# Kernel tuning notes

Hardware: AMD Instinct MI355X
Metric: run time of the kernel (lower is better)

Reference implementation:

```python
import jax, jax.numpy as jnp
import numpy as np

N, HID, MAXD, B, NCLS, GRUH = 50000, 128, 16, 50, 10, 32


def setup_inputs() -> dict:
    key = jax.random.key(0)
    ks = jax.random.split(key, 18)
    s = 0.05
    nrm = lambda k, shp: (jax.random.normal(k, shp, jnp.float32) * s)
    return {
        "feature": jax.random.normal(ks[0], (N, HID), jnp.float32),
        "nbr_idx": jax.random.randint(ks[1], (N, MAXD), 0, N, dtype=jnp.int32),
        "deg": jax.random.randint(ks[2], (N,), 1, MAXD + 1, dtype=jnp.int32),
        "graph_ids": (jnp.arange(N, dtype=jnp.int32) * B) // N,
        # SAGEConv(lstm) params: LSTM(in=HID, hidden=HID) + fc_self/fc_neigh
        "lstm_Wih": nrm(ks[3], (4 * HID, HID)),
        "lstm_Whh": nrm(ks[4], (4 * HID, HID)),
        "lstm_bih": nrm(ks[5], (4 * HID,)),
        "lstm_bhh": nrm(ks[6], (4 * HID,)),
        "W_self": nrm(ks[7], (HID, HID)),
        "W_neigh": nrm(ks[8], (HID, HID)),
        "b_sage": nrm(ks[9], (HID,)),
        # GraphConv params
        "W_gc": nrm(ks[10], (HID, HID)),
        "b_gc": nrm(ks[11], (HID,)),
        # GRU params (h0=0 so weight_hh contributes nothing; only its bias matters)
        "Wih_gru": nrm(ks[12], (3 * GRUH, HID)),
        "bih_gru": nrm(ks[13], (3 * GRUH,)),
        "bhh_gru": nrm(ks[14], (3 * GRUH,)),
        # classifier (dropout is identity at eval)
        "W_cls": nrm(ks[15], (GRUH, NCLS)),
        "b_cls": nrm(ks[16], (NCLS,)),
    }


def _lstm_aggregate(feats, nbr_idx, deg, Wih, Whh, bih, bhh):
    # DGL SAGEConv 'lstm' reducer: run LSTM over each node's neighbor features,
    # take final hidden state. Implemented as a masked scan over padded lists.
    n, hdim = feats.shape
    h0 = jnp.zeros((n, hdim), feats.dtype)

    def step(carry, t):
        h, c = carry
        x = feats[jnp.take(nbr_idx, t, axis=1)]  # [N, HID] gather of t-th neighbor
        gates = x @ Wih.T + bih + h @ Whh.T + bhh
        i, f, g, o = jnp.split(gates, 4, axis=-1)  # torch gate order i,f,g,o
        c_new = jax.nn.sigmoid(f) * c + jax.nn.sigmoid(i) * jnp.tanh(g)
        h_new = jax.nn.sigmoid(o) * jnp.tanh(c_new)
        valid = (t < deg)[:, None]
        return (jnp.where(valid, h_new, h), jnp.where(valid, c_new, c)), None

    (hT, _), _ = jax.lax.scan(step, (h0, h0), jnp.arange(nbr_idx.shape[1]))
    return hT  # hidden at each node's last valid neighbor


def _graph_conv(h, nbr_idx, deg, W, b):
    # DGL GraphConv norm='both': D^-1/2 A D^-1/2 h W + b
    n, maxd = nbr_idx.shape
    norm = jax.lax.rsqrt(jnp.maximum(deg.astype(h.dtype), 1.0))
    hn = h * norm[:, None]
    mask = (jnp.arange(maxd, dtype=jnp.int32)[None, :] < deg[:, None]).astype(h.dtype)
    contrib = hn[nbr_idx.reshape(-1)] * mask.reshape(-1)[:, None]  # [N*MAXD, HID]
    dst = jnp.repeat(jnp.arange(n, dtype=jnp.int32), maxd)
    agg = jax.ops.segment_sum(contrib, dst, num_segments=n)
    return (agg * norm[:, None]) @ W + b


def _gru_step(x, Wih, bih, bhh):
    # single GRU step with h0 = 0 (seq_len == 1 in the original view(1, N, H))
    gh = x @ Wih.T + bih  # [N, 3*GRUH]
    xr, xz, xn = jnp.split(gh, 3, axis=-1)  # torch gate order r,z,n
    br, bz, bn = jnp.split(bhh, 3)
    r = jax.nn.sigmoid(xr + br)
    z = jax.nn.sigmoid(xz + bz)
    nst = jnp.tanh(xn + r * bn)
    return (1.0 - z) * nst  # h' = (1-z)*n + z*h0, h0 = 0


def reference(feature, nbr_idx, deg, graph_ids, lstm_Wih, lstm_Whh, lstm_bih,
              lstm_bhh, W_self, W_neigh, b_sage, W_gc, b_gc, Wih_gru, bih_gru,
              bhh_gru, W_cls, b_cls):
    # conv4: SAGEConv lstm -> relu
    h_nei = _lstm_aggregate(feature, nbr_idx, deg, lstm_Wih, lstm_Whh, lstm_bih, lstm_bhh)
    h = jax.nn.relu(feature @ W_self + h_nei @ W_neigh + b_sage)
    # conv2: GraphConv -> relu
    h = jax.nn.relu(_graph_conv(h, nbr_idx, deg, W_gc, b_gc))
    # GRU over seq_len=1, batch=N
    out = _gru_step(h, Wih_gru, bih_gru, bhh_gru)  # [N, 32]
    # dgl.mean_nodes: per-graph mean pool
    sums = jax.ops.segment_sum(out, graph_ids, num_segments=B)
    cnts = jax.ops.segment_sum(jnp.ones((out.shape[0],), out.dtype), graph_ids, num_segments=B)
    hg = sums / cnts[:, None]
    # classify (Dropout is identity in eval)
    return hg @ W_cls + b_cls  # [B, NCLS]
```

## Files before the change

### kernel.cpp

```cpp
#include <hip/hip_runtime.h>
#include <hip/hip_bf16.h>


#define NN     50000
#define HIDD   128
#define MAXD   16
#define NGRAPH 50
#define NCLSS  10
#define GRUH   32

typedef __attribute__((ext_vector_type(8))) short s16x8;
typedef __attribute__((ext_vector_type(4))) float f32x4;
typedef __hip_bfloat16 bf16;

#define MFMA16(a,b,c)  __builtin_amdgcn_mfma_f32_16x16x32_bf16((a),(b),(c),0,0,0)

__device__ __forceinline__ float bf2f(bf16 x) { return __bfloat162float(x); }
__device__ __forceinline__ bf16  f2bf(float x) { return __float2bfloat16(x); }
__device__ __forceinline__ s16x8 ldfrag(const bf16* p) { return *(const s16x8*)p; }

__device__ __forceinline__ float sigf(float x) {
  return __builtin_amdgcn_rcpf(1.0f + __expf(-x));
}
__device__ __forceinline__ float tanhf_(float x) {
  return 1.0f - 2.0f * __builtin_amdgcn_rcpf(1.0f + __expf(2.0f * x));
}

__device__ __forceinline__ void lgkm_barrier() {
  asm volatile("s_waitcnt lgkmcnt(0)\n\ts_barrier" ::: "memory");
}

__global__ void prep_kernel(const float* __restrict__ feat, const float* __restrict__ Wih,
                            const float* __restrict__ Whh, const float* __restrict__ bih,
                            const float* __restrict__ bhh, const float* __restrict__ Wself,
                            const float* __restrict__ Wneigh, const float* __restrict__ Wgc,
                            const float* __restrict__ Wgru,
                            bf16* featB, bf16* WihB, bf16* WhhB, bf16* WsT, bf16* WnT,
                            bf16* WgT, bf16* WgruB, float* biasS) {
  const int nf = NN * HIDD;
  const int total = nf + 2 * 65536 + 3 * 16384 + 12288 + 512;
  int stride = gridDim.x * blockDim.x;
  for (int idx = blockIdx.x * blockDim.x + threadIdx.x; idx < total; idx += stride) {
    if (idx < nf) { featB[idx] = f2bf(feat[idx]); continue; }
    int j = idx - nf;
    if (j < 65536) { WihB[j] = f2bf(Wih[j]); continue; }
    j -= 65536;
    if (j < 65536) { WhhB[j] = f2bf(Whh[j]); continue; }
    j -= 65536;
    if (j < 16384) { int c = j >> 7, k = j & 127; WsT[j] = f2bf(Wself[k * HIDD + c]); continue; }
    j -= 16384;
    if (j < 16384) { int c = j >> 7, k = j & 127; WnT[j] = f2bf(Wneigh[k * HIDD + c]); continue; }
    j -= 16384;
    if (j < 16384) { int c = j >> 7, k = j & 127; WgT[j] = f2bf(Wgc[k * HIDD + c]); continue; }
    j -= 16384;
    if (j < 12288) { WgruB[j] = f2bf(Wgru[j]); continue; }
    j -= 12288;
    biasS[j] = bih[j] + bhh[j];
  }
}

__global__ __launch_bounds__(256) void hist_kernel(const int* __restrict__ deg, int* hist) {
  __shared__ int lh[17];
  const int tid = threadIdx.x;
  if (tid < 17) lh[tid] = 0;
  __syncthreads();
  const int i = blockIdx.x * 256 + tid;
  if (i < NN) atomicAdd(&lh[deg[i]], 1);
  __syncthreads();
  if (tid < 17 && lh[tid]) atomicAdd(&hist[tid], lh[tid]);
}

__global__ __launch_bounds__(256) void scatter_kernel(const int* __restrict__ deg,
                                                      const int* __restrict__ hist,
                                                      int* __restrict__ resv,
                                                      int* __restrict__ perm) {
  __shared__ int lh[17], lbase[17], lpos[17];
  const int tid = threadIdx.x;
  if (tid < 17) { lh[tid] = 0; lpos[tid] = 0; }
  __syncthreads();
  const int i = blockIdx.x * 256 + tid;
  const int d = (i < NN) ? deg[i] : -1;
  if (d >= 0) atomicAdd(&lh[d], 1);
  __syncthreads();
  if (tid < 17) {
    int pre = 0;
    for (int k = tid + 1; k < 17; ++k) pre += hist[k];
    lbase[tid] = pre + (lh[tid] ? atomicAdd(&resv[tid], lh[tid]) : 0);
  }
  __syncthreads();
  if (d >= 0) {
    const int p = lbase[d] + atomicAdd(&lpos[d], 1);
    perm[p] = i;
  }
}

__global__ __launch_bounds__(512, 1) void lstm_kernel(const bf16* __restrict__ featB,
                                                      const bf16* __restrict__ WihB,
                                                      const bf16* __restrict__ WhhB,
                                                      const float* __restrict__ biasS,
                                                      const int* __restrict__ nbr_idx,
                                                      const int* __restrict__ deg,
                                                      const int* __restrict__ perm,
                                                      bf16* __restrict__ hTB) {
  __shared__ __align__(16) bf16 WiA[512 * 64];
  __shared__ __align__(16) bf16 WiB[384 * 64];
  __shared__ __align__(16) bf16 Xs[2][32 * 128];
  __shared__ __align__(16) bf16 Hs[2][32 * 128];
  __shared__ int nbr_s[16 * 32];
  __shared__ int nodes_s[32];
  __shared__ int degs_s[32];

  const int tid = threadIdx.x;
  const int lane = tid & 63, w = tid >> 6;
  const int l15 = lane & 15, quad = lane >> 4;
  const int base = blockIdx.x * 32;
  const int colw = w * 16 + l15;
  const int srow = tid >> 4, schk = tid & 15;

  if (tid < 32) {
    const int gi = base + tid;
    const int nd = (gi < NN) ? perm[gi] : -1;
    nodes_s[tid] = nd;
    degs_s[tid] = (nd >= 0) ? deg[nd] : 0;
  }
  __syncthreads();
  for (int e = tid; e < 16 * 32; e += 512) {
    const int row = e & 31, t = e >> 5;
    const int nd = nodes_s[row];
    nbr_s[t * 32 + row] = (nd >= 0) ? nbr_idx[nd * MAXD + t] : 0;
  }
  {
    const int c = tid;
#pragma unroll
    for (int j = 0; j < 8; ++j)
      *(s16x8*)(WiA + c * 64 + ((j ^ (c & 7)) * 8)) = ldfrag(WihB + c * HIDD + j * 8);
    if (c < 384) {
#pragma unroll
      for (int j = 0; j < 8; ++j)
        *(s16x8*)(WiB + c * 64 + ((j ^ (c & 7)) * 8)) = ldfrag(WihB + c * HIDD + 64 + j * 8);
    }
  }

  s16x8 Bh[4][4], BiR[2];
#pragma unroll
  for (int q = 0; q < 4; ++q)
#pragma unroll
    for (int kt = 0; kt < 4; ++kt) {
      Bh[q][kt] = ldfrag(WhhB + (q * 128 + colw) * HIDD + kt * 32 + quad * 8);
      asm volatile("" : "+v"(Bh[q][kt]));
    }
#pragma unroll
  for (int kt = 2; kt < 4; ++kt) {
    BiR[kt - 2] = ldfrag(WihB + (3 * 128 + colw) * HIDD + kt * 32 + quad * 8);
    asm volatile("" : "+v"(BiR[kt - 2]));
  }
  float biasv[4];
#pragma unroll
  for (int q = 0; q < 4; ++q) biasv[q] = biasS[q * 128 + colw];

  __syncthreads();
  const int maxdeg = degs_s[0];

  int mydeg[2][4];
#pragma unroll
  for (int rt = 0; rt < 2; ++rt)
#pragma unroll
    for (int rr = 0; rr < 4; ++rr) mydeg[rt][rr] = degs_s[rt * 16 + quad * 4 + rr];

  {
    const int nb0 = nbr_s[0 * 32 + srow];
    *(s16x8*)(Xs[0] + srow * 128 + ((schk ^ (srow & 15)) * 8)) =
        ldfrag(featB + (size_t)nb0 * HIDD + schk * 8);
  }
  float cst[2][4] = {{0.f, 0.f, 0.f, 0.f}, {0.f, 0.f, 0.f, 0.f}};
  float hprev[2][4] = {{0.f, 0.f, 0.f, 0.f}, {0.f, 0.f, 0.f, 0.f}};
  lgkm_barrier();

  for (int t = 0; t < maxdeg; ++t) {
    const int cur = t & 1, nxt = cur ^ 1;
    s16x8 xstage;
    const bool do_stage = (t + 1 < maxdeg);
    if (do_stage) {
      const int nb1 = nbr_s[(t + 1) * 32 + srow];
      xstage = ldfrag(featB + (size_t)nb1 * HIDD + schk * 8);
    }

    f32x4 acc[2][4];
#pragma unroll
    for (int rt = 0; rt < 2; ++rt)
#pragma unroll
      for (int q = 0; q < 4; ++q) acc[rt][q] = (f32x4){0.f, 0.f, 0.f, 0.f};

#pragma unroll
    for (int kt = 0; kt < 4; ++kt) {
      const int oct = kt * 4 + quad;
      const int o8 = (kt & 1) * 4 + quad;
      const s16x8 ax0 = ldfrag(Xs[cur] + (0 * 16 + l15) * 128 + ((oct ^ l15) * 8));
      const s16x8 ax1 = ldfrag(Xs[cur] + (1 * 16 + l15) * 128 + ((oct ^ l15) * 8));
#pragma unroll
      for (int q = 0; q < 4; ++q) {
        const int col = q * 128 + colw;
        s16x8 bi;
        if (kt < 2)      bi = ldfrag(WiA + col * 64 + ((o8 ^ (col & 7)) * 8));
        else if (q < 3)  bi = ldfrag(WiB + col * 64 + ((o8 ^ (col & 7)) * 8));
        else             bi = BiR[kt - 2];
        acc[0][q] = MFMA16(ax0, bi, acc[0][q]);
        acc[1][q] = MFMA16(ax1, bi, acc[1][q]);
      }
    }

    if (t > 0) {
#pragma unroll
      for (int rt = 0; rt < 2; ++rt)
#pragma unroll
        for (int kt = 0; kt < 4; ++kt) {
          const int m = rt * 16 + l15;
          const int oct = kt * 4 + quad;
          const s16x8 ah = ldfrag(Hs[cur] + m * 128 + ((oct ^ l15) * 8));
#pragma unroll
          for (int q = 0; q < 4; ++q)
            acc[rt][q] = MFMA16(ah, Bh[q][kt], acc[rt][q]);
        }
    }

#pragma unroll
    for (int rt = 0; rt < 2; ++rt)
#pragma unroll
      for (int rr = 0; rr < 4; ++rr) {
        const int row = rt * 16 + quad * 4 + rr;
        const float g_i = acc[rt][0][rr] + biasv[0];
        const float g_f = acc[rt][1][rr] + biasv[1];
        const float g_g = acc[rt][2][rr] + biasv[2];
        const float g_o = acc[rt][3][rr] + biasv[3];
        const float iv = sigf(g_i), fv = sigf(g_f);
        const float gv = tanhf_(g_g), ov = sigf(g_o);
        const float cn = fv * cst[rt][rr] + iv * gv;
        const float hn_new = ov * tanhf_(cn);
        const bool act = (t < mydeg[rt][rr]);
        if (act) cst[rt][rr] = cn;
        const float hn = act ? hn_new : hprev[rt][rr];
        hprev[rt][rr] = hn;
        Hs[nxt][row * 128 + (((colw >> 3) ^ (row & 15)) * 8) + (colw & 7)] = f2bf(hn);
      }
    if (do_stage)
      *(s16x8*)(Xs[nxt] + srow * 128 + ((schk ^ (srow & 15)) * 8)) = xstage;

    lgkm_barrier();
  }

  const bf16* Hf = Hs[maxdeg & 1];
  for (int e = tid; e < 32 * 16; e += 512) {
    const int row = e >> 4, j = e & 15;
    const int nd = nodes_s[row];
    if (nd >= 0) {
      const s16x8 v = ldfrag(Hf + row * 128 + ((j ^ (row & 15)) * 8));
      *(s16x8*)(hTB + (size_t)nd * HIDD + j * 8) = v;
    }
  }
}

__global__ __launch_bounds__(256) void sage_kernel(const bf16* __restrict__ featB,
                                                   const bf16* __restrict__ hTB,
                                                   const bf16* __restrict__ WsT,
                                                   const bf16* __restrict__ WnT,
                                                   const float* __restrict__ b_sage,
                                                   const int* __restrict__ deg,
                                                   bf16* __restrict__ h1n) {
  const int lane = threadIdx.x & 63, wave = threadIdx.x >> 6;
  const int l15 = lane & 15, quad = lane >> 4;
  const int nb = blockIdx.x * 64 + wave * 16;
  int arow = nb + l15; if (arow >= NN) arow = NN - 1;
  s16x8 Fa[4], Ha[4];
#pragma unroll
  for (int kt = 0; kt < 4; ++kt) {
    Fa[kt] = ldfrag(featB + (size_t)arow * HIDD + kt * 32 + quad * 8);
    Ha[kt] = ldfrag(hTB + (size_t)arow * HIDD + kt * 32 + quad * 8);
  }
  int nodes[4]; float nrm[4];
#pragma unroll
  for (int r = 0; r < 4; ++r) {
    const int nd = nb + quad * 4 + r;
    nodes[r] = nd;
    nrm[r] = rsqrtf((float)deg[(nd < NN) ? nd : (NN - 1)]);
  }
  for (int ct = 0; ct < 8; ++ct) {
    const int col = ct * 16 + l15;
    f32x4 acc = {0.f, 0.f, 0.f, 0.f};
#pragma unroll
    for (int kt = 0; kt < 4; ++kt) {
      acc = MFMA16(Fa[kt], ldfrag(WsT + col * HIDD + kt * 32 + quad * 8), acc);
      acc = MFMA16(Ha[kt], ldfrag(WnT + col * HIDD + kt * 32 + quad * 8), acc);
    }
    const float bb = b_sage[col];
#pragma unroll
    for (int r = 0; r < 4; ++r)
      if (nodes[r] < NN) {
        const float v = fmaxf(acc[r] + bb, 0.f) * nrm[r];
        h1n[(size_t)nodes[r] * HIDD + col] = f2bf(v);
      }
  }
}

__global__ __launch_bounds__(256) void agg_kernel(const bf16* __restrict__ h1n,
                                                  const int* __restrict__ nbr_idx,
                                                  const int* __restrict__ deg,
                                                  bf16* __restrict__ aggB) {
  const int wave = threadIdx.x >> 6, lane = threadIdx.x & 63;
  const int node = blockIdx.x * 4 + wave;
  if (node >= NN) return;
  const int d = deg[node];
  const int idx_l = nbr_idx[node * MAXD + (lane & 15)];
  const int c = lane * 2;
  float a0 = 0.f, a1 = 0.f;
  for (int t = 0; t < d; ++t) {
    const int nbr = __shfl(idx_l, t, 64);
    const __hip_bfloat162 v = *(const __hip_bfloat162*)(h1n + (size_t)nbr * HIDD + c);
    a0 += __bfloat162float(v.x);
    a1 += __bfloat162float(v.y);
  }
  const float nm = rsqrtf((float)d);
  aggB[(size_t)node * HIDD + c]     = f2bf(a0 * nm);
  aggB[(size_t)node * HIDD + c + 1] = f2bf(a1 * nm);
}

__global__ __launch_bounds__(256) void gcgru_kernel(const bf16* __restrict__ aggB,
                                                    const bf16* __restrict__ WgT,
                                                    const float* __restrict__ b_gc,
                                                    const bf16* __restrict__ WgruB,
                                                    const float* __restrict__ bih,
                                                    const float* __restrict__ bhh,
                                                    float* __restrict__ gout) {
  __shared__ __align__(16) bf16 H2[64 * 136];
  const int lane = threadIdx.x & 63, wave = threadIdx.x >> 6;
  const int l15 = lane & 15, quad = lane >> 4;
  const int nb = blockIdx.x * 64 + wave * 16;
  int arow = nb + l15; if (arow >= NN) arow = NN - 1;
  s16x8 A[4];
#pragma unroll
  for (int kt = 0; kt < 4; ++kt) A[kt] = ldfrag(aggB + (size_t)arow * HIDD + kt * 32 + quad * 8);
  for (int ct = 0; ct < 8; ++ct) {
    const int col = ct * 16 + l15;
    f32x4 acc = {0.f, 0.f, 0.f, 0.f};
#pragma unroll
    for (int kt = 0; kt < 4; ++kt)
      acc = MFMA16(A[kt], ldfrag(WgT + col * HIDD + kt * 32 + quad * 8), acc);
    const float bb = b_gc[col];
#pragma unroll
    for (int r = 0; r < 4; ++r)
      H2[(wave * 16 + quad * 4 + r) * 136 + col] = f2bf(fmaxf(acc[r] + bb, 0.f));
  }
  __syncthreads();
  s16x8 A2[4];
#pragma unroll
  for (int kt = 0; kt < 4; ++kt)
    A2[kt] = ldfrag(H2 + (wave * 16 + l15) * 136 + kt * 32 + quad * 8);
  f32x4 acc[6];
#pragma unroll
  for (int ct = 0; ct < 6; ++ct) {
    f32x4 a = {0.f, 0.f, 0.f, 0.f};
#pragma unroll
    for (int kt = 0; kt < 4; ++kt)
      a = MFMA16(A2[kt], ldfrag(WgruB + (ct * 16 + l15) * HIDD + kt * 32 + quad * 8), a);
    acc[ct] = a;
  }
#pragma unroll
  for (int u = 0; u < 2; ++u) {
    const int cu = 16 * u + l15;
    const float br = bih[cu] + bhh[cu];
    const float bz = bih[32 + cu] + bhh[32 + cu];
    const float bni = bih[64 + cu];
    const float bnh = bhh[64 + cu];
#pragma unroll
    for (int r = 0; r < 4; ++r) {
      const int node = nb + quad * 4 + r;
      if (node < NN) {
        const float rv = sigf(acc[u][r] + br);
        const float zv = sigf(acc[2 + u][r] + bz);
        const float nv = tanhf_(acc[4 + u][r] + bni + rv * bnh);
        gout[(size_t)node * GRUH + cu] = (1.f - zv) * nv;
      }
    }
  }
}

#define POOL_CHUNK 512
__global__ __launch_bounds__(256) void pool_partial_kernel(const float* __restrict__ gout,
                                                           const int* __restrict__ gids,
                                                           float* __restrict__ sums,
                                                           float* __restrict__ cnts) {
  __shared__ float ls[NGRAPH * GRUH];
  __shared__ float lc[NGRAPH];
  const int tid = threadIdx.x;
  for (int i = tid; i < NGRAPH * GRUH; i += 256) ls[i] = 0.f;
  if (tid < NGRAPH) lc[tid] = 0.f;
  __syncthreads();

  const int wave = tid >> 6, lane = tid & 63;
  const int c = lane & 31, half = lane >> 5;
  const int base = blockIdx.x * POOL_CHUNK + wave * (POOL_CHUNK / 8);

  float accv = 0.f, ccnt = 0.f;
  int curg = -1;
  for (int it = 0; it < POOL_CHUNK / 16; ++it) {
    const int n = base + it * 2 + half;
    if (n < NN) {
      const int g = gids[n];
      const float v = gout[(size_t)n * GRUH + c];
      if (g != curg) {
        if (curg >= 0) {
          atomicAdd(&ls[curg * GRUH + c], accv);
          if (c == 0) atomicAdd(&lc[curg], ccnt);
        }
        curg = g; accv = 0.f; ccnt = 0.f;
      }
      accv += v; ccnt += 1.f;
    }
  }
  if (curg >= 0) {
    atomicAdd(&ls[curg * GRUH + c], accv);
    if (c == 0) atomicAdd(&lc[curg], ccnt);
  }
  __syncthreads();
  for (int i = tid; i < NGRAPH * GRUH; i += 256)
    if (ls[i] != 0.f) atomicAdd(&sums[i], ls[i]);
  if (tid < NGRAPH && lc[tid] != 0.f) atomicAdd(&cnts[tid], lc[tid]);
}

__global__ __launch_bounds__(256) void pool_final_kernel(const float* __restrict__ sums,
                                                         const float* __restrict__ cnts,
                                                         const float* __restrict__ Wcls,
                                                         const float* __restrict__ bcls,
                                                         float* __restrict__ out) {
  const int idx = blockIdx.x * blockDim.x + threadIdx.x;
  if (idx >= NGRAPH * NCLSS) return;
  const int g = idx / NCLSS, k = idx % NCLSS;
  const float inv = 1.0f / cnts[g];
  float acc = bcls[k];
#pragma unroll
  for (int cc = 0; cc < GRUH; ++cc)
    acc += sums[g * GRUH + cc] * inv * Wcls[cc * NCLSS + k];
  out[idx] = acc;
}

extern "C" void kernel_launch(void* const* d_in, const int* in_sizes, int n_in,
                              void* d_out, int out_size, void* d_ws, size_t ws_size,
                              hipStream_t stream) {
  const float* feature  = (const float*)d_in[0];
  const int*   nbr_idx  = (const int*)d_in[1];
  const int*   deg      = (const int*)d_in[2];
  const int*   gids     = (const int*)d_in[3];
  const float* lstm_Wih = (const float*)d_in[4];
  const float* lstm_Whh = (const float*)d_in[5];
  const float* lstm_bih = (const float*)d_in[6];
  const float* lstm_bhh = (const float*)d_in[7];
  const float* W_self   = (const float*)d_in[8];
  const float* W_neigh  = (const float*)d_in[9];
  const float* b_sage   = (const float*)d_in[10];
  const float* W_gc     = (const float*)d_in[11];
  const float* b_gc     = (const float*)d_in[12];
  const float* Wih_gru  = (const float*)d_in[13];
  const float* bih_gru  = (const float*)d_in[14];
  const float* bhh_gru  = (const float*)d_in[15];
  const float* W_cls    = (const float*)d_in[16];
  const float* b_cls    = (const float*)d_in[17];

  char* ws = (char*)d_ws;
  bf16*  featB = (bf16*)(ws + 0);
  bf16*  hTB   = (bf16*)(ws + 12800000);
  bf16*  h1nB  = (bf16*)(ws + 25600000);
  bf16*  aggB  = (bf16*)(ws + 38400000);
  float* gout  = (float*)(ws + 12800000);
  const size_t wo = 64000000;
  bf16*  WihB  = (bf16*)(ws + wo);
  bf16*  WhhB  = (bf16*)(ws + wo + 131072);
  bf16*  WsT   = (bf16*)(ws + wo + 262144);
  bf16*  WnT   = (bf16*)(ws + wo + 294912);
  bf16*  WgT   = (bf16*)(ws + wo + 327680);
  bf16*  WgruB = (bf16*)(ws + wo + 360448);
  float* biasS = (float*)(ws + wo + 385024);
  int*   perm  = (int*)(ws + 65000000);
  int*   hist  = (int*)(ws + 65400000);
  int*   resv  = hist + 17;
  float* psums = (float*)(ws + 65401216);
  float* pcnts = psums + NGRAPH * GRUH;

  prep_kernel<<<3072, 256, 0, stream>>>(feature, lstm_Wih, lstm_Whh, lstm_bih, lstm_bhh,
                                        W_self, W_neigh, W_gc, Wih_gru,
                                        featB, WihB, WhhB, WsT, WnT, WgT, WgruB, biasS);
  hipMemsetAsync(hist, 0, 34 * sizeof(int), stream);
  hipMemsetAsync(psums, 0, (NGRAPH * GRUH + NGRAPH) * sizeof(float), stream);
  hist_kernel<<<196, 256, 0, stream>>>(deg, hist);
  scatter_kernel<<<196, 256, 0, stream>>>(deg, hist, resv, perm);
  lstm_kernel<<<1563, 512, 0, stream>>>(featB, WihB, WhhB, biasS, nbr_idx, deg, perm, hTB);
  sage_kernel<<<782, 256, 0, stream>>>(featB, hTB, WsT, WnT, b_sage, deg, h1nB);
  agg_kernel<<<12500, 256, 0, stream>>>(h1nB, nbr_idx, deg, aggB);
  gcgru_kernel<<<782, 256, 0, stream>>>(aggB, WgT, b_gc, WgruB, bih_gru, bhh_gru, gout);
  pool_partial_kernel<<<(NN + POOL_CHUNK - 1) / POOL_CHUNK, 256, 0, stream>>>(gout, gids, psums, pcnts);
  pool_final_kernel<<<2, 256, 0, stream>>>(psums, pcnts, W_cls, b_cls, (float*)d_out);
}
```

Measured before the change: 429.7 us.

## Process 64 nodes per LSTM block and single-buffer X/H tiles

Doubles the LSTM kernel's row tile from 32 to 64 nodes per block, so each weight fragment loaded from LDS or registers feeds four MFMAs instead of two and the launch needs half as many blocks. Double-buffered Xs/Hs are replaced by single buffers, with an extra barrier between the matmul reads and the writes of the next X stage and the new H. The hidden state is now written to LDS only for active rows, which removes the hprev registers. The cost is more accumulator registers (64 floats), an extra barrier per step, and fewer blocks to spread across CUs.

Result: slower. 446.7 us (+4.0%).

```diff
diff --git a/kernel.cpp b/kernel.cpp
--- a/kernel.cpp
+++ b/kernel.cpp
@@ -104,30 +104,30 @@
                                                       bf16* __restrict__ hTB) {
   __shared__ __align__(16) bf16 WiA[512 * 64];
   __shared__ __align__(16) bf16 WiB[384 * 64];
-  __shared__ __align__(16) bf16 Xs[2][32 * 128];
-  __shared__ __align__(16) bf16 Hs[2][32 * 128];
-  __shared__ int nbr_s[16 * 32];
-  __shared__ int nodes_s[32];
-  __shared__ int degs_s[32];
+  __shared__ __align__(16) bf16 Xs[64 * 128];
+  __shared__ __align__(16) bf16 Hs[64 * 128];
+  __shared__ int nbr_s[16 * 64];
+  __shared__ int nodes_s[64];
+  __shared__ int degs_s[64];
 
   const int tid = threadIdx.x;
   const int lane = tid & 63, w = tid >> 6;
   const int l15 = lane & 15, quad = lane >> 4;
-  const int base = blockIdx.x * 32;
+  const int base = blockIdx.x * 64;
   const int colw = w * 16 + l15;
   const int srow = tid >> 4, schk = tid & 15;
 
-  if (tid < 32) {
+  if (tid < 64) {
     const int gi = base + tid;
     const int nd = (gi < NN) ? perm[gi] : -1;
     nodes_s[tid] = nd;
     degs_s[tid] = (nd >= 0) ? deg[nd] : 0;
   }
   __syncthreads();
-  for (int e = tid; e < 16 * 32; e += 512) {
-    const int row = e & 31, t = e >> 5;
+  for (int e = tid; e < 16 * 64; e += 512) {
+    const int row = e & 63, t = e >> 6;
     const int nd = nodes_s[row];
-    nbr_s[t * 32 + row] = (nd >= 0) ? nbr_idx[nd * MAXD + t] : 0;
+    nbr_s[t * 64 + row] = (nd >= 0) ? nbr_idx[nd * MAXD + t] : 0;
   }
   {
     const int c = tid;
@@ -161,33 +161,40 @@
   __syncthreads();
   const int maxdeg = degs_s[0];
 
-  int mydeg[2][4];
-#pragma unroll
-  for (int rt = 0; rt < 2; ++rt)
+  int mydeg[4][4];
+#pragma unroll
+  for (int rt = 0; rt < 4; ++rt)
 #pragma unroll
     for (int rr = 0; rr < 4; ++rr) mydeg[rt][rr] = degs_s[rt * 16 + quad * 4 + rr];
 
   {
-    const int nb0 = nbr_s[0 * 32 + srow];
-    *(s16x8*)(Xs[0] + srow * 128 + ((schk ^ (srow & 15)) * 8)) =
-        ldfrag(featB + (size_t)nb0 * HIDD + schk * 8);
-  }
-  float cst[2][4] = {{0.f, 0.f, 0.f, 0.f}, {0.f, 0.f, 0.f, 0.f}};
-  float hprev[2][4] = {{0.f, 0.f, 0.f, 0.f}, {0.f, 0.f, 0.f, 0.f}};
+    const int na = nbr_s[0 * 64 + srow];
+    const int nb2 = nbr_s[0 * 64 + srow + 32];
+    *(s16x8*)(Xs + srow * 128 + ((schk ^ (srow & 15)) * 8)) =
+        ldfrag(featB + (size_t)na * HIDD + schk * 8);
+    *(s16x8*)(Xs + (srow + 32) * 128 + ((schk ^ ((srow + 32) & 15)) * 8)) =
+        ldfrag(featB + (size_t)nb2 * HIDD + schk * 8);
+  }
+  float cst[4][4];
+#pragma unroll
+  for (int rt = 0; rt < 4; ++rt)
+#pragma unroll
+    for (int rr = 0; rr < 4; ++rr) cst[rt][rr] = 0.f;
   lgkm_barrier();
 
   for (int t = 0; t < maxdeg; ++t) {
-    const int cur = t & 1, nxt = cur ^ 1;
-    s16x8 xstage;
+    s16x8 xstage0, xstage1;
     const bool do_stage = (t + 1 < maxdeg);
     if (do_stage) {
-      const int nb1 = nbr_s[(t + 1) * 32 + srow];
-      xstage = ldfrag(featB + (size_t)nb1 * HIDD + schk * 8);
-    }
-
-    f32x4 acc[2][4];
-#pragma unroll
-    for (int rt = 0; rt < 2; ++rt)
+      const int na = nbr_s[(t + 1) * 64 + srow];
+      const int nb2 = nbr_s[(t + 1) * 64 + srow + 32];
+      xstage0 = ldfrag(featB + (size_t)na * HIDD + schk * 8);
+      xstage1 = ldfrag(featB + (size_t)nb2 * HIDD + schk * 8);
+    }
+
+    f32x4 acc[4][4];
+#pragma unroll
+    for (int rt = 0; rt < 4; ++rt)
 #pragma unroll
       for (int q = 0; q < 4; ++q) acc[rt][q] = (f32x4){0.f, 0.f, 0.f, 0.f};
 
@@ -195,8 +202,12 @@
     for (int kt = 0; kt < 4; ++kt) {
       const int oct = kt * 4 + quad;
       const int o8 = (kt & 1) * 4 + quad;
-      const s16x8 ax0 = ldfrag(Xs[cur] + (0 * 16 + l15) * 128 + ((oct ^ l15) * 8));
-      const s16x8 ax1 = ldfrag(Xs[cur] + (1 * 16 + l15) * 128 + ((oct ^ l15) * 8));
+      s16x8 ax[4];
+#pragma unroll
+      for (int rt = 0; rt < 4; ++rt) {
+        const int m = rt * 16 + l15;
+        ax[rt] = ldfrag(Xs + m * 128 + ((oct ^ (m & 15)) * 8));
+      }
 #pragma unroll
       for (int q = 0; q < 4; ++q) {
         const int col = q * 128 + colw;
@@ -204,27 +215,35 @@
         if (kt < 2)      bi = ldfrag(WiA + col * 64 + ((o8 ^ (col & 7)) * 8));
         else if (q < 3)  bi = ldfrag(WiB + col * 64 + ((o8 ^ (col & 7)) * 8));
         else             bi = BiR[kt - 2];
-        acc[0][q] = MFMA16(ax0, bi, acc[0][q]);
-        acc[1][q] = MFMA16(ax1, bi, acc[1][q]);
+#pragma unroll
+        for (int rt = 0; rt < 4; ++rt)
+          acc[rt][q] = MFMA16(ax[rt], bi, acc[rt][q]);
       }
     }
 
     if (t > 0) {
 #pragma unroll
-      for (int rt = 0; rt < 2; ++rt)
-#pragma unroll
-        for (int kt = 0; kt < 4; ++kt) {
+      for (int kt = 0; kt < 4; ++kt) {
+        const int oct = kt * 4 + quad;
+#pragma unroll
+        for (int rt = 0; rt < 4; ++rt) {
           const int m = rt * 16 + l15;
-          const int oct = kt * 4 + quad;
-          const s16x8 ah = ldfrag(Hs[cur] + m * 128 + ((oct ^ l15) * 8));
+          const s16x8 ah = ldfrag(Hs + m * 128 + ((oct ^ (m & 15)) * 8));
 #pragma unroll
           for (int q = 0; q < 4; ++q)
             acc[rt][q] = MFMA16(ah, Bh[q][kt], acc[rt][q]);
         }
-    }
-
-#pragma unroll
-    for (int rt = 0; rt < 2; ++rt)
+      }
+    }
+    lgkm_barrier();
+
+    if (do_stage) {
+      *(s16x8*)(Xs + srow * 128 + ((schk ^ (srow & 15)) * 8)) = xstage0;
+      *(s16x8*)(Xs + (srow + 32) * 128 + ((schk ^ ((srow + 32) & 15)) * 8)) = xstage1;
+    }
+
+#pragma unroll
+    for (int rt = 0; rt < 4; ++rt)
 #pragma unroll
       for (int rr = 0; rr < 4; ++rr) {
         const int row = rt * 16 + quad * 4 + rr;
@@ -235,25 +254,20 @@
         const float iv = sigf(g_i), fv = sigf(g_f);
         const float gv = tanhf_(g_g), ov = sigf(g_o);
         const float cn = fv * cst[rt][rr] + iv * gv;
-        const float hn_new = ov * tanhf_(cn);
-        const bool act = (t < mydeg[rt][rr]);
-        if (act) cst[rt][rr] = cn;
-        const float hn = act ? hn_new : hprev[rt][rr];
-        hprev[rt][rr] = hn;
-        Hs[nxt][row * 128 + (((colw >> 3) ^ (row & 15)) * 8) + (colw & 7)] = f2bf(hn);
-      }
-    if (do_stage)
-      *(s16x8*)(Xs[nxt] + srow * 128 + ((schk ^ (srow & 15)) * 8)) = xstage;
-
+        const float hn = ov * tanhf_(cn);
+        if (t < mydeg[rt][rr]) {
+          cst[rt][rr] = cn;
+          Hs[row * 128 + (((colw >> 3) ^ (row & 15)) * 8) + (colw & 7)] = f2bf(hn);
+        }
+      }
     lgkm_barrier();
   }
 
-  const bf16* Hf = Hs[maxdeg & 1];
-  for (int e = tid; e < 32 * 16; e += 512) {
+  for (int e = tid; e < 64 * 16; e += 512) {
     const int row = e >> 4, j = e & 15;
     const int nd = nodes_s[row];
     if (nd >= 0) {
-      const s16x8 v = ldfrag(Hf + row * 128 + ((j ^ (row & 15)) * 8));
+      const s16x8 v = ldfrag(Hs + row * 128 + ((j ^ (row & 15)) * 8));
       *(s16x8*)(hTB + (size_t)nd * HIDD + j * 8) = v;
     }
   }
@@ -491,7 +505,7 @@
   hipMemsetAsync(psums, 0, (NGRAPH * GRUH + NGRAPH) * sizeof(float), stream);
   hist_kernel<<<196, 256, 0, stream>>>(deg, hist);
   scatter_kernel<<<196, 256, 0, stream>>>(deg, hist, resv, perm);
-  lstm_kernel<<<1563, 512, 0, stream>>>(featB, WihB, WhhB, biasS, nbr_idx, deg, perm, hTB);
+  lstm_kernel<<<(NN + 63) / 64, 512, 0, stream>>>(featB, WihB, WhhB, biasS, nbr_idx, deg, perm, hTB);
   sage_kernel<<<782, 256, 0, stream>>>(featB, hTB, WsT, WnT, b_sage, deg, h1nB);
   agg_kernel<<<12500, 256, 0, stream>>>(h1nB, nbr_idx, deg, aggB);
   gcgru_kernel<<<782, 256, 0, stream>>>(aggB, WgT, b_gc, WgruB, bih_gru, bhh_gru, gout);
```
